# Performance work log

Measured on AMD Instinct MI355X. Metric: run time of the kernel, lower is better.

The kernel has to match this reference:

```python
import jax, jax.numpy as jnp
import numpy as np

BN_EPS = 1e-5

def _square_distance(src, dst):
    # src [B,N,3], dst [B,S,3] -> [B,N,S]
    d = -2.0 * jnp.einsum('bnc,bsc->bns', src, dst)
    d = d + jnp.sum(src * src, -1)[:, :, None]
    d = d + jnp.sum(dst * dst, -1)[:, None, :]
    return d

def _conv_bn_relu(x, w, b, g, beta):
    # x [B,C,N]; 1x1 conv == channel GEMM, then training-mode batchnorm over (B,N)
    y = jnp.einsum('oc,bcn->bon', w, x) + b[None, :, None]
    mean = jnp.mean(y, axis=(0, 2), keepdims=True)
    var = jnp.mean((y - mean) ** 2, axis=(0, 2), keepdims=True)  # biased, as torch BN uses for normalization
    y = (y - mean) * jax.lax.rsqrt(var + BN_EPS)
    y = y * g[None, :, None] + beta[None, :, None]
    return jax.nn.relu(y)

def setup_inputs() -> dict:
    key = jax.random.key(0)
    ks = jax.random.split(key, 8)
    B, N, S, D1, D2 = 8, 8192, 2048, 128, 256
    C_in, C_mid, C_out = D1 + D2, 256, 256
    return {
        'xyz1': jax.random.normal(ks[0], (B, 3, N), jnp.float32),
        'xyz2': jax.random.normal(ks[1], (B, 3, S), jnp.float32),
        'points1': jax.random.normal(ks[2], (B, D1, N), jnp.float32),
        'points2': jax.random.normal(ks[3], (B, D2, S), jnp.float32),
        'w1': jax.random.normal(ks[4], (C_mid, C_in), jnp.float32) * (1.0 / np.sqrt(C_in)),
        'b1': jax.random.normal(ks[5], (C_mid,), jnp.float32) * 0.01,
        'g1': jnp.ones((C_mid,), jnp.float32),
        'beta1': jnp.zeros((C_mid,), jnp.float32),
        'w2': jax.random.normal(ks[6], (C_out, C_mid), jnp.float32) * (1.0 / np.sqrt(C_mid)),
        'b2': jax.random.normal(ks[7], (C_out,), jnp.float32) * 0.01,
        'g2': jnp.ones((C_out,), jnp.float32),
        'beta2': jnp.zeros((C_out,), jnp.float32),
    }

def reference(xyz1, xyz2, points1, points2, w1, b1, g1, beta1, w2, b2, g2, beta2):
    B = xyz1.shape[0]
    p1xyz = jnp.transpose(xyz1, (0, 2, 1))      # [B,N,3]
    p2xyz = jnp.transpose(xyz2, (0, 2, 1))      # [B,S,3]
    p2 = jnp.transpose(points2, (0, 2, 1))      # [B,S,D2]

    dists = _square_distance(p1xyz, p2xyz)      # [B,N,S]
    neg_d3, idx = jax.lax.top_k(-dists, 3)      # 3 smallest distances
    d3 = -neg_d3                                # [B,N,3]
    recip = 1.0 / (d3 + 1e-8)
    weight = recip / jnp.sum(recip, axis=2, keepdims=True)  # [B,N,3]

    gathered = jax.vmap(lambda p, i: p[i])(p2, idx)          # [B,N,3,D2]
    interp = jnp.sum(gathered * weight[..., None], axis=2)   # [B,N,D2]

    new_points = jnp.concatenate([jnp.transpose(points1, (0, 2, 1)), interp], axis=-1)
    x = jnp.transpose(new_points, (0, 2, 1))    # [B,D1+D2,N]
    x = _conv_bn_relu(x, w1, b1, g1, beta1)
    x = _conv_bn_relu(x, w2, b2, g2, beta2)
    return x
```

## Files before the change

kernel.cpp:

```cpp
#include <hip/hip_runtime.h>

#define B_    8
#define N_    8192
#define S_    2048
#define D1_   128
#define D2_   256
#define CIN_  384
#define CMID_ 256
#define COUT_ 256

typedef unsigned int  u32;
typedef unsigned short u16;
typedef __attribute__((ext_vector_type(8))) short short8;
typedef __attribute__((ext_vector_type(4))) float f32x4;

static __device__ __forceinline__ u32 uminu(u32 a, u32 b) { return a < b ? a : b; }
static __device__ __forceinline__ u32 umaxu(u32 a, u32 b) { return a > b ? a : b; }
static __device__ __forceinline__ u32 umed3(u32 a, u32 b, u32 c) {
  u32 d;
  asm("v_med3_u32 %0, %1, %2, %3" : "=v"(d) : "v"(a), "v"(b), "v"(c));
  return d;
}
static __device__ __forceinline__ u16 f2bf(float f) {
  union { float f; u32 u; } v; v.f = f;
  u32 r = v.u + 0x7FFFu + ((v.u >> 16) & 1u);
  return (u16)(r >> 16);
}
static __device__ __forceinline__ float bflo(u32 u) { return __uint_as_float(u << 16); }
static __device__ __forceinline__ float bfhi(u32 u) { return __uint_as_float(u & 0xFFFF0000u); }
static __device__ __forceinline__ u32 cvtpk_bf16(float lo, float hi) {
  u32 d;
  asm("v_cvt_pk_bf16_f32 %0, %1, %2" : "=v"(d) : "v"(lo), "v"(hi));
  return d;
}

#define GLD16(g, l)                                                             \
  __builtin_amdgcn_global_load_lds((const __attribute__((address_space(1))) void*)(g), \
                                   (__attribute__((address_space(3))) void*)(l), 16, 0, 0)

__global__ __launch_bounds__(256) void k_prep(const float* __restrict__ xyz2,
                                              float4* __restrict__ pts4) {
  const int b = blockIdx.y, s = blockIdx.x * 256 + threadIdx.x;
  const float* xb = xyz2 + (size_t)b * 3 * S_;
  float x = xb[s], y = xb[S_ + s], z = xb[2 * S_ + s];
  pts4[b * S_ + s] = make_float4(-2.f * x, -2.f * y, -2.f * z, x * x + y * y + z * z);
}

__global__ __launch_bounds__(256) void k_nn_scan(const float* __restrict__ xyz1,
                                                 const float4* __restrict__ pts4,
                                                 uint4* __restrict__ keys) {
  const int b = blockIdx.z, chunk = blockIdx.y;
  const int n = blockIdx.x * 256 + threadIdx.x;
  const float* pb = xyz1 + (size_t)b * 3 * N_;
  const float px = pb[n], py = pb[N_ + n], pz = pb[2 * N_ + n];
  const float pn = px * px + py * py + pz * pz;
  const float4* __restrict__ P = pts4 + b * S_ + chunk * 256;
  u32 m0 = ~0u, m1 = ~0u, m2 = ~0u, m3 = ~0u;
#pragma unroll 8
  for (int s = 0; s < 256; ++s) {
    float4 q = P[s];
    float d = fmaf(px, q.x, fmaf(py, q.y, fmaf(pz, q.z, pn + q.w)));
    d = fmaxf(d, 0.f);
    u32 k = (__float_as_uint(d) & 0xFFFFFF00u) | (u32)s;
    m3 = uminu(m3, umaxu(m2, k));
    m2 = umed3(m1, m2, k);
    m1 = umed3(m0, m1, k);
    m0 = uminu(m0, k);
  }
  uint4 v; v.x = m0; v.y = m1; v.z = m2; v.w = m3;
  keys[((size_t)(b * 8 + chunk)) * N_ + n] = v;
}

__global__ __launch_bounds__(256) void k_refine(const float* __restrict__ xyz1,
                                                const float4* __restrict__ pts4,
                                                const uint4* __restrict__ keys,
                                                int4* __restrict__ idx4,
                                                float4* __restrict__ w4) {
  const int b = blockIdx.y, n = blockIdx.x * 256 + threadIdx.x;
  const float* pb = xyz1 + (size_t)b * 3 * N_;
  const double px = (double)pb[n], py = (double)pb[N_ + n], pz = (double)pb[2 * N_ + n];
  const double pn = px * px + py * py + pz * pz;
  double bd0 = 1e300, bd1 = 1e300, bd2 = 1e300;
  int bi0 = 1 << 30, bi1 = 1 << 30, bi2 = 1 << 30;
#pragma unroll
  for (int c = 0; c < 8; ++c) {
    uint4 kk = keys[((size_t)(b * 8 + c)) * N_ + n];
    u32 arr[4] = {kk.x, kk.y, kk.z, kk.w};
#pragma unroll
    for (int j = 0; j < 4; ++j) {
      int s = c * 256 + (int)(arr[j] & 255u);
      float4 q = pts4[b * S_ + s];
      double x = (double)(q.x * -0.5f), y = (double)(q.y * -0.5f), z = (double)(q.z * -0.5f);
      double dot = px * x + py * y + pz * z;
      double d = -2.0 * dot + (pn + (x * x + y * y + z * z));
      if (d < bd2 || (d == bd2 && s < bi2)) {
        if (d < bd1 || (d == bd1 && s < bi1)) {
          bd2 = bd1; bi2 = bi1;
          if (d < bd0 || (d == bd0 && s < bi0)) { bd1 = bd0; bi1 = bi0; bd0 = d; bi0 = s; }
          else                                  { bd1 = d;  bi1 = s; }
        } else { bd2 = d; bi2 = s; }
      }
    }
  }
  float f0 = (float)bd0, f1 = (float)bd1, f2 = (float)bd2;
  float r0 = 1.f / (f0 + 1e-8f), r1 = 1.f / (f1 + 1e-8f), r2 = 1.f / (f2 + 1e-8f);
  float rs = r0 + r1 + r2;
  w4[(size_t)b * N_ + n]   = make_float4(r0 / rs, r1 / rs, r2 / rs, 0.f);
  idx4[(size_t)b * N_ + n] = make_int4(bi0, bi1, bi2, 0);
}

__global__ __launch_bounds__(256) void k_p2t(const float* __restrict__ p2,
                                             float* __restrict__ p2T) {
  __shared__ float t[32][33];
  const int b = blockIdx.z, s0 = blockIdx.x * 32, d0 = blockIdx.y * 32;
  const int cc = threadIdx.x & 31, rr = threadIdx.x >> 5;
#pragma unroll
  for (int i = 0; i < 4; ++i) {
    int r = rr + i * 8;
    t[r][cc] = p2[((size_t)b * D2_ + d0 + r) * S_ + s0 + cc];
  }
  __syncthreads();
#pragma unroll
  for (int i = 0; i < 4; ++i) {
    int r = rr + i * 8;
    p2T[((size_t)b * S_ + s0 + r) * D2_ + d0 + cc] = t[cc][r];
  }
}

__global__ __launch_bounds__(256) void k_packp1(const float* __restrict__ p1,
                                                u16* __restrict__ xT) {
  __shared__ float t[32][33];
  const int b = blockIdx.z, n0 = blockIdx.x * 32, c0 = blockIdx.y * 32;
  const int cc = threadIdx.x & 31, rr = threadIdx.x >> 5;
#pragma unroll
  for (int i = 0; i < 4; ++i) {
    int r = rr + i * 8;
    t[r][cc] = p1[((size_t)b * D1_ + c0 + r) * N_ + n0 + cc];
  }
  __syncthreads();
#pragma unroll
  for (int i = 0; i < 4; ++i) {
    int r = rr + i * 8;
    xT[((size_t)b * N_ + n0 + r) * CIN_ + c0 + cc] = f2bf(t[cc][r]);
  }
}

__global__ __launch_bounds__(256) void k_gather_pack(const float* __restrict__ p2T,
                                                     const int4* __restrict__ idx4,
                                                     const float4* __restrict__ w4,
                                                     u16* __restrict__ xT) {
  const int b = blockIdx.y;
  const int wv = threadIdx.x >> 6, lane = threadIdx.x & 63;
  const int nbase = blockIdx.x * 16 + wv * 4;
  int4   id[4];
  float4 w[4];
#pragma unroll
  for (int i = 0; i < 4; ++i) {
    id[i] = idx4[(size_t)b * N_ + nbase + i];
    w[i]  = w4[(size_t)b * N_ + nbase + i];
  }
#pragma unroll
  for (int i = 0; i < 4; ++i) {
    const int n = nbase + i;
    const float4* r0 = (const float4*)(p2T + ((size_t)b * S_ + id[i].x) * D2_) + lane;
    const float4* r1 = (const float4*)(p2T + ((size_t)b * S_ + id[i].y) * D2_) + lane;
    const float4* r2 = (const float4*)(p2T + ((size_t)b * S_ + id[i].z) * D2_) + lane;
    float4 a = *r0, bb = *r1, cq = *r2;
    ushort4 pk;
    pk.x = f2bf(a.x * w[i].x + bb.x * w[i].y + cq.x * w[i].z);
    pk.y = f2bf(a.y * w[i].x + bb.y * w[i].y + cq.y * w[i].z);
    pk.z = f2bf(a.z * w[i].x + bb.z * w[i].y + cq.z * w[i].z);
    pk.w = f2bf(a.w * w[i].x + bb.w * w[i].y + cq.w * w[i].z);
    *(ushort4*)(xT + ((size_t)b * N_ + n) * CIN_ + D1_ + lane * 4) = pk;
  }
}

__global__ __launch_bounds__(256) void k_wcvt(const float* __restrict__ w1,
                                              const float* __restrict__ w2,
                                              u16* __restrict__ w1b,
                                              u16* __restrict__ w2b) {
  int i = blockIdx.x * 256 + threadIdx.x;
  if (i < CMID_ * CIN_) w1b[i] = f2bf(w1[i]);
  int j = i - CMID_ * CIN_;
  if (j >= 0 && j < COUT_ * CMID_) w2b[j] = f2bf(w2[j]);
}

__global__ __launch_bounds__(64) void k_bnstat(const float* __restrict__ ps,
                                               const float* __restrict__ pq,
                                               const float* __restrict__ g,
                                               const float* __restrict__ beta,
                                               float* __restrict__ scale,
                                               float* __restrict__ shift) {
  const int o = blockIdx.x, l = threadIdx.x;
  float s = 0.f, q = 0.f;
#pragma unroll
  for (int i = 0; i < 8; ++i) {
    s += ps[(size_t)o * 512 + i * 64 + l];
    q += pq[(size_t)o * 512 + i * 64 + l];
  }
#pragma unroll
  for (int m = 1; m <= 32; m <<= 1) { s += __shfl_xor(s, m); q += __shfl_xor(q, m); }
  if (l == 0) {
    const float inv = 1.0f / (float)(B_ * N_);
    float mean = s * inv;
    float var = q * inv - mean * mean;
    float sc = g[o] / sqrtf(var + 1e-5f);
    scale[o] = sc;
    shift[o] = beta[o] - mean * sc;
  }
}

__global__ __launch_bounds__(256) void k_gemm1(const u16* __restrict__ Wb,
                                               const float* __restrict__ bias,
                                               const u16* __restrict__ xT,
                                               u16* __restrict__ y1T,
                                               float* __restrict__ psum,
                                               float* __restrict__ pssq) {
  __shared__ u16 As[2][4096];
  __shared__ u16 Bs[2][4096];
  __shared__ float s_sum[128], s_ssq[128];
  const int b = blockIdx.z, bm0 = blockIdx.y * 128, bn0 = blockIdx.x * 128;
  const int tid = threadIdx.x, w = tid >> 6, l = tid & 63;
  const int wm = w & 1, wn = w >> 1;
  const int lr = l >> 2, lc = l & 3;
  const int fm = l & 15, fq = l >> 4;
  const int clog = (lc ^ ((lr >> 1) & 3)) * 8;
  const int swz8 = (fq ^ ((fm >> 1) & 3)) * 8;
  if (tid < 128) { s_sum[tid] = 0.f; s_ssq[tid] = 0.f; }
  f32x4 acc[4][4];
#pragma unroll
  for (int i = 0; i < 4; ++i)
#pragma unroll
    for (int j = 0; j < 4; ++j) acc[i][j] = (f32x4){0.f, 0.f, 0.f, 0.f};

  const int NK = CIN_ / 32;
#pragma unroll
  for (int j = 0; j < 2; ++j) {
    int seg = w * 2 + j, row = seg * 16 + lr;
    GLD16(Wb + (size_t)(bm0 + row) * CIN_ + clog, &As[0][seg * 512]);
    GLD16(xT + ((size_t)b * N_ + bn0 + row) * CIN_ + clog, &Bs[0][seg * 512]);
  }
  for (int kk = 0; kk < NK; ++kk) {
    __syncthreads();
    const int cur = kk & 1;
    if (kk + 1 < NK) {
      const int k0 = (kk + 1) * 32, nxt = cur ^ 1;
#pragma unroll
      for (int j = 0; j < 2; ++j) {
        int seg = w * 2 + j, row = seg * 16 + lr;
        GLD16(Wb + (size_t)(bm0 + row) * CIN_ + k0 + clog, &As[nxt][seg * 512]);
        GLD16(xT + ((size_t)b * N_ + bn0 + row) * CIN_ + k0 + clog, &Bs[nxt][seg * 512]);
      }
    }
    short8 af[4], bfr[4];
#pragma unroll
    for (int f = 0; f < 4; ++f) {
      af[f]  = *(const short8*)&As[cur][(wm * 64 + f * 16 + fm) * 32 + swz8];
      bfr[f] = *(const short8*)&Bs[cur][(wn * 64 + f * 16 + fm) * 32 + swz8];
    }
#pragma unroll
    for (int i = 0; i < 4; ++i)
#pragma unroll
      for (int j = 0; j < 4; ++j)
        acc[i][j] = __builtin_amdgcn_mfma_f32_16x16x32_bf16(af[i], bfr[j], acc[i][j], 0, 0, 0);
  }
  u16* tb = y1T + ((size_t)b * 64 + (bn0 >> 7)) * 32768;
#pragma unroll
  for (int i = 0; i < 4; ++i) {
    int ob = bm0 + wm * 64 + i * 16 + fq * 4;
    float4 b4 = *(const float4*)(bias + ob);
    float sv0 = 0, sv1 = 0, sv2 = 0, sv3 = 0, qv0 = 0, qv1 = 0, qv2 = 0, qv3 = 0;
#pragma unroll
    for (int j = 0; j < 4; ++j) {
      int nl = wn * 64 + j * 16 + fm;
      ushort4 pk;
      pk.x = f2bf(acc[i][j][0] + b4.x);
      pk.y = f2bf(acc[i][j][1] + b4.y);
      pk.z = f2bf(acc[i][j][2] + b4.z);
      pk.w = f2bf(acc[i][j][3] + b4.w);
      *(ushort4*)(tb + (size_t)(ob >> 5) * 4096 + nl * 32 + (ob & 31)) = pk;
      float v0 = bflo(pk.x), v1 = bflo(pk.y), v2 = bflo(pk.z), v3 = bflo(pk.w);
      sv0 += v0; sv1 += v1; sv2 += v2; sv3 += v3;
      qv0 = fmaf(v0, v0, qv0); qv1 = fmaf(v1, v1, qv1);
      qv2 = fmaf(v2, v2, qv2); qv3 = fmaf(v3, v3, qv3);
    }
#pragma unroll
    for (int m = 1; m <= 8; m <<= 1) {
      sv0 += __shfl_xor(sv0, m); sv1 += __shfl_xor(sv1, m);
      sv2 += __shfl_xor(sv2, m); sv3 += __shfl_xor(sv3, m);
      qv0 += __shfl_xor(qv0, m); qv1 += __shfl_xor(qv1, m);
      qv2 += __shfl_xor(qv2, m); qv3 += __shfl_xor(qv3, m);
    }
    if (fm == 0) {
      int ol = wm * 64 + i * 16 + fq * 4;
      atomicAdd(&s_sum[ol + 0], sv0); atomicAdd(&s_sum[ol + 1], sv1);
      atomicAdd(&s_sum[ol + 2], sv2); atomicAdd(&s_sum[ol + 3], sv3);
      atomicAdd(&s_ssq[ol + 0], qv0); atomicAdd(&s_ssq[ol + 1], qv1);
      atomicAdd(&s_ssq[ol + 2], qv2); atomicAdd(&s_ssq[ol + 3], qv3);
    }
  }
  __syncthreads();
  if (tid < 128) {
    const int blk = blockIdx.x + 64 * blockIdx.z;
    psum[(size_t)(bm0 + tid) * 512 + blk] = s_sum[tid];
    pssq[(size_t)(bm0 + tid) * 512 + blk] = s_ssq[tid];
  }
}

__global__ __launch_bounds__(256) void k_gemm2(const u16* __restrict__ Wb2,
                                               const float* __restrict__ b2,
                                               const u16* __restrict__ y1T,
                                               const float* __restrict__ scale,
                                               const float* __restrict__ shift,
                                               u16* __restrict__ y2T,
                                               float* __restrict__ psum,
                                               float* __restrict__ pssq) {
  __shared__ u16 As[2][4096];
  __shared__ u16 Bs[2][4096];
  __shared__ float s_sum[128], s_ssq[128];
  __shared__ float s_sc[CMID_], s_sh[CMID_];
  const int b = blockIdx.z, bm0 = blockIdx.y * 128, bn0 = blockIdx.x * 128;
  const int tid = threadIdx.x, w = tid >> 6, l = tid & 63;
  const int wm = w & 1, wn = w >> 1;
  const int lr = l >> 2, lc = l & 3;
  const int fm = l & 15, fq = l >> 4;
  const int clog = (lc ^ ((lr >> 1) & 3)) * 8;
  const int swz8 = (fq ^ ((fm >> 1) & 3)) * 8;
  if (tid < 128) { s_sum[tid] = 0.f; s_ssq[tid] = 0.f; }
  s_sc[tid] = scale[tid];
  s_sh[tid] = shift[tid];
  f32x4 acc[4][4];
#pragma unroll
  for (int i = 0; i < 4; ++i)
#pragma unroll
    for (int j = 0; j < 4; ++j) acc[i][j] = (f32x4){0.f, 0.f, 0.f, 0.f};

  const u16* tb = y1T + ((size_t)b * 64 + (bn0 >> 7)) * 32768;
  const int NK = CMID_ / 32;
#pragma unroll
  for (int j = 0; j < 2; ++j) {
    int seg = w * 2 + j, row = seg * 16 + lr;
    GLD16(Wb2 + (size_t)(bm0 + row) * CMID_ + clog, &As[0][seg * 512]);
    GLD16(tb + row * 32 + clog, &Bs[0][seg * 512]);
  }
  for (int kk = 0; kk < NK; ++kk) {
    __syncthreads();
    const int cur = kk & 1;
    if (kk + 1 < NK) {
      const int nxt = cur ^ 1;
#pragma unroll
      for (int j = 0; j < 2; ++j) {
        int seg = w * 2 + j, row = seg * 16 + lr;
        GLD16(Wb2 + (size_t)(bm0 + row) * CMID_ + (kk + 1) * 32 + clog, &As[nxt][seg * 512]);
        GLD16(tb + (size_t)(kk + 1) * 4096 + row * 32 + clog, &Bs[nxt][seg * 512]);
      }
    }
    const int kb = kk * 32 + fq * 8;
    float4 s0 = *(const float4*)&s_sc[kb], s1 = *(const float4*)&s_sc[kb + 4];
    float4 h0 = *(const float4*)&s_sh[kb], h1 = *(const float4*)&s_sh[kb + 4];
    short8 af[4], bfr[4];
#pragma unroll
    for (int f = 0; f < 4; ++f) {
      af[f] = *(const short8*)&As[cur][(wm * 64 + f * 16 + fm) * 32 + swz8];
      uint4 r = *(const uint4*)&Bs[cur][(wn * 64 + f * 16 + fm) * 32 + swz8];
      float v0 = fmaxf(fmaf(bflo(r.x), s0.x, h0.x), 0.f);
      float v1 = fmaxf(fmaf(bfhi(r.x), s0.y, h0.y), 0.f);
      float v2 = fmaxf(fmaf(bflo(r.y), s0.z, h0.z), 0.f);
      float v3 = fmaxf(fmaf(bfhi(r.y), s0.w, h0.w), 0.f);
      float v4 = fmaxf(fmaf(bflo(r.z), s1.x, h1.x), 0.f);
      float v5 = fmaxf(fmaf(bfhi(r.z), s1.y, h1.y), 0.f);
      float v6 = fmaxf(fmaf(bflo(r.w), s1.z, h1.z), 0.f);
      float v7 = fmaxf(fmaf(bfhi(r.w), s1.w, h1.w), 0.f);
      union { u32 u[4]; short8 s; } cv;
      cv.u[0] = cvtpk_bf16(v0, v1); cv.u[1] = cvtpk_bf16(v2, v3);
      cv.u[2] = cvtpk_bf16(v4, v5); cv.u[3] = cvtpk_bf16(v6, v7);
      bfr[f] = cv.s;
    }
#pragma unroll
    for (int i = 0; i < 4; ++i)
#pragma unroll
      for (int j = 0; j < 4; ++j)
        acc[i][j] = __builtin_amdgcn_mfma_f32_16x16x32_bf16(af[i], bfr[j], acc[i][j], 0, 0, 0);
  }
  u16* tb2 = y2T + ((size_t)b * 64 + (bn0 >> 7)) * 32768;
#pragma unroll
  for (int i = 0; i < 4; ++i) {
    int ob = bm0 + wm * 64 + i * 16 + fq * 4;
    float4 b4 = *(const float4*)(b2 + ob);
    float sv0 = 0, sv1 = 0, sv2 = 0, sv3 = 0, qv0 = 0, qv1 = 0, qv2 = 0, qv3 = 0;
#pragma unroll
    for (int j = 0; j < 4; ++j) {
      int nl = wn * 64 + j * 16 + fm;
      ushort4 pk;
      pk.x = f2bf(acc[i][j][0] + b4.x);
      pk.y = f2bf(acc[i][j][1] + b4.y);
      pk.z = f2bf(acc[i][j][2] + b4.z);
      pk.w = f2bf(acc[i][j][3] + b4.w);
      *(ushort4*)(tb2 + (size_t)(ob >> 5) * 4096 + nl * 32 + (ob & 31)) = pk;
      float v0 = bflo(pk.x), v1 = bflo(pk.y), v2 = bflo(pk.z), v3 = bflo(pk.w);
      sv0 += v0; sv1 += v1; sv2 += v2; sv3 += v3;
      qv0 = fmaf(v0, v0, qv0); qv1 = fmaf(v1, v1, qv1);
      qv2 = fmaf(v2, v2, qv2); qv3 = fmaf(v3, v3, qv3);
    }
#pragma unroll
    for (int m = 1; m <= 8; m <<= 1) {
      sv0 += __shfl_xor(sv0, m); sv1 += __shfl_xor(sv1, m);
      sv2 += __shfl_xor(sv2, m); sv3 += __shfl_xor(sv3, m);
      qv0 += __shfl_xor(qv0, m); qv1 += __shfl_xor(qv1, m);
      qv2 += __shfl_xor(qv2, m); qv3 += __shfl_xor(qv3, m);
    }
    if (fm == 0) {
      int ol = wm * 64 + i * 16 + fq * 4;
      atomicAdd(&s_sum[ol + 0], sv0); atomicAdd(&s_sum[ol + 1], sv1);
      atomicAdd(&s_sum[ol + 2], sv2); atomicAdd(&s_sum[ol + 3], sv3);
      atomicAdd(&s_ssq[ol + 0], qv0); atomicAdd(&s_ssq[ol + 1], qv1);
      atomicAdd(&s_ssq[ol + 2], qv2); atomicAdd(&s_ssq[ol + 3], qv3);
    }
  }
  __syncthreads();
  if (tid < 128) {
    const int blk = blockIdx.x + 64 * blockIdx.z;
    psum[(size_t)(bm0 + tid) * 512 + blk] = s_sum[tid];
    pssq[(size_t)(bm0 + tid) * 512 + blk] = s_ssq[tid];
  }
}

__global__ __launch_bounds__(256) void k_bn2t(const u16* __restrict__ y2T,
                                              const float* __restrict__ scale,
                                              const float* __restrict__ shift,
                                              float* __restrict__ out) {
  __shared__ float t[32][33];
  const int b = blockIdx.z, n0 = blockIdx.x * 32, o0 = blockIdx.y * 32;
  const int cc = threadIdx.x & 31, rr = threadIdx.x >> 5;
  const float sc = scale[o0 + cc], sh = shift[o0 + cc];
  const u16* tb = y2T + ((size_t)b * 64 + (n0 >> 7)) * 32768 +
                  (size_t)(o0 >> 5) * 4096 + (size_t)(n0 & 96) * 32;
#pragma unroll
  for (int i = 0; i < 4; ++i) {
    int r = rr + i * 8;
    float v = bflo((u32)tb[r * 32 + cc]);
    t[r][cc] = fmaxf(fmaf(v, sc, sh), 0.f);
  }
  __syncthreads();
#pragma unroll
  for (int i = 0; i < 4; ++i) {
    int r = rr + i * 8;
    out[((size_t)b * COUT_ + o0 + r) * N_ + n0 + cc] = t[cc][r];
  }
}

extern "C" void kernel_launch(void* const* d_in, const int* in_sizes, int n_in,
                              void* d_out, int out_size, void* d_ws, size_t ws_size,
                              hipStream_t stream) {
  const float* xyz1    = (const float*)d_in[0];
  const float* xyz2    = (const float*)d_in[1];
  const float* points1 = (const float*)d_in[2];
  const float* points2 = (const float*)d_in[3];
  const float* w1      = (const float*)d_in[4];
  const float* b1      = (const float*)d_in[5];
  const float* g1      = (const float*)d_in[6];
  const float* beta1   = (const float*)d_in[7];
  const float* w2      = (const float*)d_in[8];
  const float* b2      = (const float*)d_in[9];
  const float* g2      = (const float*)d_in[10];
  const float* beta2   = (const float*)d_in[11];
  float* out = (float*)d_out;

  char* ws = (char*)d_ws;
  size_t off = 0;
  u16*    xT    = (u16*)(ws + off);    off += (size_t)B_ * N_ * CIN_ * 2;
  u16*    y1T   = (u16*)(ws + off);    off += (size_t)B_ * N_ * CMID_ * 2;
  float*  p2T   = (float*)(ws + off);  off += (size_t)B_ * S_ * D2_ * 4;
  float4* pts4  = (float4*)(ws + off); off += (size_t)B_ * S_ * 16;
  uint4*  keys  = (uint4*)(ws + off);  off += (size_t)B_ * 8 * N_ * 16;
  int4*   idx4  = (int4*)(ws + off);   off += (size_t)B_ * N_ * 16;
  float4* w4    = (float4*)(ws + off); off += (size_t)B_ * N_ * 16;
  u16*    w1b   = (u16*)(ws + off);    off += (size_t)CMID_ * CIN_ * 2;
  u16*    w2b   = (u16*)(ws + off);    off += (size_t)COUT_ * CMID_ * 2;
  float*  stats = (float*)(ws + off);
  u16*    y2T   = xT;
  float* psum1 = (float*)keys;
  float* pssq1 = psum1 + 256 * 512;
  float* psum2 = pssq1 + 256 * 512;
  float* pssq2 = psum2 + 256 * 512;
  float* scale1 = stats,        * shift1 = stats + 256;
  float* scale2 = stats + 512,  * shift2 = stats + 768;

  k_wcvt       <<<dim3((CMID_ * CIN_ + COUT_ * CMID_) / 256), 256, 0, stream>>>(w1, w2, w1b, w2b);
  k_prep       <<<dim3(S_ / 256, B_), 256, 0, stream>>>(xyz2, pts4);
  k_p2t        <<<dim3(S_ / 32, D2_ / 32, B_), 256, 0, stream>>>(points2, p2T);
  k_nn_scan    <<<dim3(N_ / 256, 8, B_), 256, 0, stream>>>(xyz1, pts4, keys);
  k_refine     <<<dim3(N_ / 256, B_), 256, 0, stream>>>(xyz1, pts4, keys, idx4, w4);
  k_packp1     <<<dim3(N_ / 32, D1_ / 32, B_), 256, 0, stream>>>(points1, xT);
  k_gather_pack<<<dim3(N_ / 16, B_), 256, 0, stream>>>(p2T, idx4, w4, xT);
  k_gemm1      <<<dim3(N_ / 128, CMID_ / 128, B_), 256, 0, stream>>>(w1b, b1, xT, y1T,
                                                                     psum1, pssq1);
  k_bnstat     <<<dim3(CMID_), 64, 0, stream>>>(psum1, pssq1, g1, beta1, scale1, shift1);
  k_gemm2      <<<dim3(N_ / 128, COUT_ / 128, B_), 256, 0, stream>>>(w2b, b2, y1T,
                                                                     scale1, shift1,
                                                                     y2T, psum2, pssq2);
  k_bnstat     <<<dim3(COUT_), 64, 0, stream>>>(psum2, pssq2, g2, beta2, scale2, shift2);
  k_bn2t       <<<dim3(N_ / 32, COUT_ / 32, B_), 256, 0, stream>>>(y2T, scale2, shift2, out);
}
```

Baseline: 287.1 us.

## Widen GEMM tiles to full output channels, trim NN candidates, merge prep kernels

Both 1x1-conv GEMMs now use 512-thread blocks that cover all 256 output channels per 128-point tile. Each point tile of the activation matrix is therefore loaded once instead of twice, and half as many blocks are launched. The nearest-neighbour scan now keeps 3 candidates per chunk instead of 4, which cuts min/med3 work in the scan and distance evaluations in the refine pass. This relies on the 24-bit key truncation not pushing the true third neighbour out of a chunk's top three. The weight conversion and point preprocessing kernels are merged into one launch to save launch overhead.

```diff
diff --git a/kernel.cpp b/kernel.cpp
--- a/kernel.cpp
+++ b/kernel.cpp
@@ -38,12 +38,24 @@
   __builtin_amdgcn_global_load_lds((const __attribute__((address_space(1))) void*)(g), \
                                    (__attribute__((address_space(3))) void*)(l), 16, 0, 0)
 
-__global__ __launch_bounds__(256) void k_prep(const float* __restrict__ xyz2,
-                                              float4* __restrict__ pts4) {
-  const int b = blockIdx.y, s = blockIdx.x * 256 + threadIdx.x;
-  const float* xb = xyz2 + (size_t)b * 3 * S_;
-  float x = xb[s], y = xb[S_ + s], z = xb[2 * S_ + s];
-  pts4[b * S_ + s] = make_float4(-2.f * x, -2.f * y, -2.f * z, x * x + y * y + z * z);
+__global__ __launch_bounds__(256) void k_pre(const float* __restrict__ xyz2,
+                                             float4* __restrict__ pts4,
+                                             const float* __restrict__ w1,
+                                             const float* __restrict__ w2,
+                                             u16* __restrict__ w1b,
+                                             u16* __restrict__ w2b) {
+  const int i = blockIdx.x * 256 + threadIdx.x;
+  if (i < B_ * S_) {
+    const int b = i >> 11, s = i & (S_ - 1);
+    const float* xb = xyz2 + (size_t)b * 3 * S_;
+    float x = xb[s], y = xb[S_ + s], z = xb[2 * S_ + s];
+    pts4[b * S_ + s] = make_float4(-2.f * x, -2.f * y, -2.f * z, x * x + y * y + z * z);
+    return;
+  }
+  const int j = i - B_ * S_;
+  if (j < CMID_ * CIN_) { w1b[j] = f2bf(w1[j]); return; }
+  const int h = j - CMID_ * CIN_;
+  if (h < COUT_ * CMID_) w2b[h] = f2bf(w2[h]);
 }
 
 __global__ __launch_bounds__(256) void k_nn_scan(const float* __restrict__ xyz1,
@@ -55,19 +67,19 @@
   const float px = pb[n], py = pb[N_ + n], pz = pb[2 * N_ + n];
   const float pn = px * px + py * py + pz * pz;
   const float4* __restrict__ P = pts4 + b * S_ + chunk * 256;
-  u32 m0 = ~0u, m1 = ~0u, m2 = ~0u, m3 = ~0u;
+  u32 m0 = ~0u, m1 = ~0u, m2 = ~0u;
 #pragma unroll 8
   for (int s = 0; s < 256; ++s) {
     float4 q = P[s];
     float d = fmaf(px, q.x, fmaf(py, q.y, fmaf(pz, q.z, pn + q.w)));
     d = fmaxf(d, 0.f);
     u32 k = (__float_as_uint(d) & 0xFFFFFF00u) | (u32)s;
-    m3 = uminu(m3, umaxu(m2, k));
-    m2 = umed3(m1, m2, k);
+    u32 t = umaxu(m1, k);
     m1 = umed3(m0, m1, k);
+    m2 = uminu(m2, t);
     m0 = uminu(m0, k);
   }
-  uint4 v; v.x = m0; v.y = m1; v.z = m2; v.w = m3;
+  uint4 v; v.x = m0; v.y = m1; v.z = m2; v.w = m2;
   keys[((size_t)(b * 8 + chunk)) * N_ + n] = v;
 }
 
@@ -85,9 +97,9 @@
 #pragma unroll
   for (int c = 0; c < 8; ++c) {
     uint4 kk = keys[((size_t)(b * 8 + c)) * N_ + n];
-    u32 arr[4] = {kk.x, kk.y, kk.z, kk.w};
-#pragma unroll
-    for (int j = 0; j < 4; ++j) {
+    u32 arr[3] = {kk.x, kk.y, kk.z};
+#pragma unroll
+    for (int j = 0; j < 3; ++j) {
       int s = c * 256 + (int)(arr[j] & 255u);
       float4 q = pts4[b * S_ + s];
       double x = (double)(q.x * -0.5f), y = (double)(q.y * -0.5f), z = (double)(q.z * -0.5f);
@@ -175,16 +187,6 @@
   }
 }
 
-__global__ __launch_bounds__(256) void k_wcvt(const float* __restrict__ w1,
-                                              const float* __restrict__ w2,
-                                              u16* __restrict__ w1b,
-                                              u16* __restrict__ w2b) {
-  int i = blockIdx.x * 256 + threadIdx.x;
-  if (i < CMID_ * CIN_) w1b[i] = f2bf(w1[i]);
-  int j = i - CMID_ * CIN_;
-  if (j >= 0 && j < COUT_ * CMID_) w2b[j] = f2bf(w2[j]);
-}
-
 __global__ __launch_bounds__(64) void k_bnstat(const float* __restrict__ ps,
                                                const float* __restrict__ pq,
                                                const float* __restrict__ g,
@@ -210,23 +212,23 @@
   }
 }
 
-__global__ __launch_bounds__(256) void k_gemm1(const u16* __restrict__ Wb,
+__global__ __launch_bounds__(512) void k_gemm1(const u16* __restrict__ Wb,
                                                const float* __restrict__ bias,
                                                const u16* __restrict__ xT,
                                                u16* __restrict__ y1T,
                                                float* __restrict__ psum,
                                                float* __restrict__ pssq) {
-  __shared__ u16 As[2][4096];
+  __shared__ u16 As[2][8192];
   __shared__ u16 Bs[2][4096];
-  __shared__ float s_sum[128], s_ssq[128];
-  const int b = blockIdx.z, bm0 = blockIdx.y * 128, bn0 = blockIdx.x * 128;
+  __shared__ float s_sum[256], s_ssq[256];
+  const int b = blockIdx.z, bn0 = blockIdx.x * 128;
   const int tid = threadIdx.x, w = tid >> 6, l = tid & 63;
-  const int wm = w & 1, wn = w >> 1;
+  const int wm = w & 3, wn = w >> 2;
   const int lr = l >> 2, lc = l & 3;
   const int fm = l & 15, fq = l >> 4;
   const int clog = (lc ^ ((lr >> 1) & 3)) * 8;
   const int swz8 = (fq ^ ((fm >> 1) & 3)) * 8;
-  if (tid < 128) { s_sum[tid] = 0.f; s_ssq[tid] = 0.f; }
+  if (tid < 256) { s_sum[tid] = 0.f; s_ssq[tid] = 0.f; }
   f32x4 acc[4][4];
 #pragma unroll
   for (int i = 0; i < 4; ++i)
@@ -237,8 +239,11 @@
 #pragma unroll
   for (int j = 0; j < 2; ++j) {
     int seg = w * 2 + j, row = seg * 16 + lr;
-    GLD16(Wb + (size_t)(bm0 + row) * CIN_ + clog, &As[0][seg * 512]);
-    GLD16(xT + ((size_t)b * N_ + bn0 + row) * CIN_ + clog, &Bs[0][seg * 512]);
+    GLD16(Wb + (size_t)row * CIN_ + clog, &As[0][seg * 512]);
+  }
+  {
+    int row = w * 16 + lr;
+    GLD16(xT + ((size_t)b * N_ + bn0 + row) * CIN_ + clog, &Bs[0][w * 512]);
   }
   for (int kk = 0; kk < NK; ++kk) {
     __syncthreads();
@@ -248,9 +253,10 @@
 #pragma unroll
       for (int j = 0; j < 2; ++j) {
         int seg = w * 2 + j, row = seg * 16 + lr;
-        GLD16(Wb + (size_t)(bm0 + row) * CIN_ + k0 + clog, &As[nxt][seg * 512]);
-        GLD16(xT + ((size_t)b * N_ + bn0 + row) * CIN_ + k0 + clog, &Bs[nxt][seg * 512]);
+        GLD16(Wb + (size_t)row * CIN_ + k0 + clog, &As[nxt][seg * 512]);
       }
+      int row = w * 16 + lr;
+      GLD16(xT + ((size_t)b * N_ + bn0 + row) * CIN_ + k0 + clog, &Bs[nxt][w * 512]);
     }
     short8 af[4], bfr[4];
 #pragma unroll
@@ -267,7 +273,7 @@
   u16* tb = y1T + ((size_t)b * 64 + (bn0 >> 7)) * 32768;
 #pragma unroll
   for (int i = 0; i < 4; ++i) {
-    int ob = bm0 + wm * 64 + i * 16 + fq * 4;
+    int ob = wm * 64 + i * 16 + fq * 4;
     float4 b4 = *(const float4*)(bias + ob);
     float sv0 = 0, sv1 = 0, sv2 = 0, sv3 = 0, qv0 = 0, qv1 = 0, qv2 = 0, qv3 = 0;
 #pragma unroll
@@ -292,22 +298,21 @@
       qv2 += __shfl_xor(qv2, m); qv3 += __shfl_xor(qv3, m);
     }
     if (fm == 0) {
-      int ol = wm * 64 + i * 16 + fq * 4;
-      atomicAdd(&s_sum[ol + 0], sv0); atomicAdd(&s_sum[ol + 1], sv1);
-      atomicAdd(&s_sum[ol + 2], sv2); atomicAdd(&s_sum[ol + 3], sv3);
-      atomicAdd(&s_ssq[ol + 0], qv0); atomicAdd(&s_ssq[ol + 1], qv1);
-      atomicAdd(&s_ssq[ol + 2], qv2); atomicAdd(&s_ssq[ol + 3], qv3);
+      atomicAdd(&s_sum[ob + 0], sv0); atomicAdd(&s_sum[ob + 1], sv1);
+      atomicAdd(&s_sum[ob + 2], sv2); atomicAdd(&s_sum[ob + 3], sv3);
+      atomicAdd(&s_ssq[ob + 0], qv0); atomicAdd(&s_ssq[ob + 1], qv1);
+      atomicAdd(&s_ssq[ob + 2], qv2); atomicAdd(&s_ssq[ob + 3], qv3);
     }
   }
   __syncthreads();
-  if (tid < 128) {
+  if (tid < 256) {
     const int blk = blockIdx.x + 64 * blockIdx.z;
-    psum[(size_t)(bm0 + tid) * 512 + blk] = s_sum[tid];
-    pssq[(size_t)(bm0 + tid) * 512 + blk] = s_ssq[tid];
-  }
-}
-
-__global__ __launch_bounds__(256) void k_gemm2(const u16* __restrict__ Wb2,
+    psum[(size_t)tid * 512 + blk] = s_sum[tid];
+    pssq[(size_t)tid * 512 + blk] = s_ssq[tid];
+  }
+}
+
+__global__ __launch_bounds__(512) void k_gemm2(const u16* __restrict__ Wb2,
                                                const float* __restrict__ b2,
                                                const u16* __restrict__ y1T,
                                                const float* __restrict__ scale,
@@ -315,20 +320,22 @@
                                                u16* __restrict__ y2T,
                                                float* __restrict__ psum,
                                                float* __restrict__ pssq) {
-  __shared__ u16 As[2][4096];
+  __shared__ u16 As[2][8192];
   __shared__ u16 Bs[2][4096];
-  __shared__ float s_sum[128], s_ssq[128];
+  __shared__ float s_sum[256], s_ssq[256];
   __shared__ float s_sc[CMID_], s_sh[CMID_];
-  const int b = blockIdx.z, bm0 = blockIdx.y * 128, bn0 = blockIdx.x * 128;
+  const int b = blockIdx.z, bn0 = blockIdx.x * 128;
   const int tid = threadIdx.x, w = tid >> 6, l = tid & 63;
-  const int wm = w & 1, wn = w >> 1;
+  const int wm = w & 3, wn = w >> 2;
   const int lr = l >> 2, lc = l & 3;
   const int fm = l & 15, fq = l >> 4;
   const int clog = (lc ^ ((lr >> 1) & 3)) * 8;
   const int swz8 = (fq ^ ((fm >> 1) & 3)) * 8;
-  if (tid < 128) { s_sum[tid] = 0.f; s_ssq[tid] = 0.f; }
-  s_sc[tid] = scale[tid];
-  s_sh[tid] = shift[tid];
+  if (tid < 256) {
+    s_sum[tid] = 0.f; s_ssq[tid] = 0.f;
+    s_sc[tid] = scale[tid];
+    s_sh[tid] = shift[tid];
+  }
   f32x4 acc[4][4];
 #pragma unroll
   for (int i = 0; i < 4; ++i)
@@ -340,8 +347,11 @@
 #pragma unroll
   for (int j = 0; j < 2; ++j) {
     int seg = w * 2 + j, row = seg * 16 + lr;
-    GLD16(Wb2 + (size_t)(bm0 + row) * CMID_ + clog, &As[0][seg * 512]);
-    GLD16(tb + row * 32 + clog, &Bs[0][seg * 512]);
+    GLD16(Wb2 + (size_t)row * CMID_ + clog, &As[0][seg * 512]);
+  }
+  {
+    int row = w * 16 + lr;
+    GLD16(tb + row * 32 + clog, &Bs[0][w * 512]);
   }
   for (int kk = 0; kk < NK; ++kk) {
     __syncthreads();
@@ -351,9 +361,10 @@
 #pragma unroll
       for (int j = 0; j < 2; ++j) {
         int seg = w * 2 + j, row = seg * 16 + lr;
-        GLD16(Wb2 + (size_t)(bm0 + row) * CMID_ + (kk + 1) * 32 + clog, &As[nxt][seg * 512]);
-        GLD16(tb + (size_t)(kk + 1) * 4096 + row * 32 + clog, &Bs[nxt][seg * 512]);
+        GLD16(Wb2 + (size_t)row * CMID_ + (kk + 1) * 32 + clog, &As[nxt][seg * 512]);
       }
+      int row = w * 16 + lr;
+      GLD16(tb + (size_t)(kk + 1) * 4096 + row * 32 + clog, &Bs[nxt][w * 512]);
     }
     const int kb = kk * 32 + fq * 8;
     float4 s0 = *(const float4*)&s_sc[kb], s1 = *(const float4*)&s_sc[kb + 4];
@@ -385,7 +396,7 @@
   u16* tb2 = y2T + ((size_t)b * 64 + (bn0 >> 7)) * 32768;
 #pragma unroll
   for (int i = 0; i < 4; ++i) {
-    int ob = bm0 + wm * 64 + i * 16 + fq * 4;
+    int ob = wm * 64 + i * 16 + fq * 4;
     float4 b4 = *(const float4*)(b2 + ob);
     float sv0 = 0, sv1 = 0, sv2 = 0, sv3 = 0, qv0 = 0, qv1 = 0, qv2 = 0, qv3 = 0;
 #pragma unroll
@@ -410,18 +421,17 @@
       qv2 += __shfl_xor(qv2, m); qv3 += __shfl_xor(qv3, m);
     }
     if (fm == 0) {
-      int ol = wm * 64 + i * 16 + fq * 4;
-      atomicAdd(&s_sum[ol + 0], sv0); atomicAdd(&s_sum[ol + 1], sv1);
-      atomicAdd(&s_sum[ol + 2], sv2); atomicAdd(&s_sum[ol + 3], sv3);
-      atomicAdd(&s_ssq[ol + 0], qv0); atomicAdd(&s_ssq[ol + 1], qv1);
-      atomicAdd(&s_ssq[ol + 2], qv2); atomicAdd(&s_ssq[ol + 3], qv3);
+      atomicAdd(&s_sum[ob + 0], sv0); atomicAdd(&s_sum[ob + 1], sv1);
+      atomicAdd(&s_sum[ob + 2], sv2); atomicAdd(&s_sum[ob + 3], sv3);
+      atomicAdd(&s_ssq[ob + 0], qv0); atomicAdd(&s_ssq[ob + 1], qv1);
+      atomicAdd(&s_ssq[ob + 2], qv2); atomicAdd(&s_ssq[ob + 3], qv3);
     }
   }
   __syncthreads();
-  if (tid < 128) {
+  if (tid < 256) {
     const int blk = blockIdx.x + 64 * blockIdx.z;
-    psum[(size_t)(bm0 + tid) * 512 + blk] = s_sum[tid];
-    pssq[(size_t)(bm0 + tid) * 512 + blk] = s_ssq[tid];
+    psum[(size_t)tid * 512 + blk] = s_sum[tid];
+    pssq[(size_t)tid * 512 + blk] = s_ssq[tid];
   }
 }
 
@@ -477,7 +487,7 @@
   float4* w4    = (float4*)(ws + off); off += (size_t)B_ * N_ * 16;
   u16*    w1b   = (u16*)(ws + off);    off += (size_t)CMID_ * CIN_ * 2;
   u16*    w2b   = (u16*)(ws + off);    off += (size_t)COUT_ * CMID_ * 2;
-  float*  stats = (float*)(ws + off);
+  float*  stats = (float*)(ws + off);  off += 1024 * sizeof(float);
   u16*    y2T   = xT;
   float* psum1 = (float*)keys;
   float* pssq1 = psum1 + 256 * 512;
@@ -486,19 +496,19 @@
   float* scale1 = stats,        * shift1 = stats + 256;
   float* scale2 = stats + 512,  * shift2 = stats + 768;
 
-  k_wcvt       <<<dim3((CMID_ * CIN_ + COUT_ * CMID_) / 256), 256, 0, stream>>>(w1, w2, w1b, w2b);
-  k_prep       <<<dim3(S_ / 256, B_), 256, 0, stream>>>(xyz2, pts4);
+  k_pre        <<<dim3((B_ * S_ + CMID_ * CIN_ + COUT_ * CMID_) / 256), 256, 0, stream>>>(
+                   xyz2, pts4, w1, w2, w1b, w2b);
   k_p2t        <<<dim3(S_ / 32, D2_ / 32, B_), 256, 0, stream>>>(points2, p2T);
   k_nn_scan    <<<dim3(N_ / 256, 8, B_), 256, 0, stream>>>(xyz1, pts4, keys);
   k_refine     <<<dim3(N_ / 256, B_), 256, 0, stream>>>(xyz1, pts4, keys, idx4, w4);
   k_packp1     <<<dim3(N_ / 32, D1_ / 32, B_), 256, 0, stream>>>(points1, xT);
   k_gather_pack<<<dim3(N_ / 16, B_), 256, 0, stream>>>(p2T, idx4, w4, xT);
-  k_gemm1      <<<dim3(N_ / 128, CMID_ / 128, B_), 256, 0, stream>>>(w1b, b1, xT, y1T,
-                                                                     psum1, pssq1);
+  k_gemm1      <<<dim3(N_ / 128, 1, B_), 512, 0, stream>>>(w1b, b1, xT, y1T,
+                                                           psum1, pssq1);
   k_bnstat     <<<dim3(CMID_), 64, 0, stream>>>(psum1, pssq1, g1, beta1, scale1, shift1);
-  k_gemm2      <<<dim3(N_ / 128, COUT_ / 128, B_), 256, 0, stream>>>(w2b, b2, y1T,
-                                                                     scale1, shift1,
-                                                                     y2T, psum2, pssq2);
+  k_gemm2      <<<dim3(N_ / 128, 1, B_), 512, 0, stream>>>(w2b, b2, y1T,
+                                                           scale1, shift1,
+                                                           y2T, psum2, pssq2);
   k_bnstat     <<<dim3(COUT_), 64, 0, stream>>>(psum2, pssq2, g2, beta2, scale2, shift2);
   k_bn2t       <<<dim3(N_ / 32, COUT_ / 32, B_), 256, 0, stream>>>(y2T, scale2, shift2, out);
 }
```

After: 271.2 us. 1.06x faster.
